# Optimization experiments

Measured on AMD Instinct MI355X. Metric: run time of the kernel, lower is better.

Reference implementation:

```python
import jax, jax.numpy as jnp
import numpy as np
from jax import lax

MAX_MEMORY_LR = 0.2
MIN_MEMORY_DECAY = 0.5
MEMORY_MAX_NORM = 15.0
NORM_EPS = 1e-6

def _inv_sig(x):
    x = max(min(x, 0.999), 0.001)
    return float(np.log(x / (1 - x)))

def setup_inputs() -> dict:
    key = jax.random.key(0)
    k1, k2 = jax.random.split(key)
    B, S, D = 16, 4096, 256
    x = jax.random.normal(k1, (B, S, D), dtype=jnp.float32)
    # xavier_uniform with gain=0.1 on (d_out, d_in)
    limit = 0.1 * float(np.sqrt(6.0 / (D + D)))
    M_init = jax.random.uniform(k2, (D, D), dtype=jnp.float32, minval=-limit, maxval=limit)
    eta_raw = jnp.asarray(_inv_sig(0.05), dtype=jnp.float32)
    alpha_raw = jnp.asarray(_inv_sig(0.9), dtype=jnp.float32)
    return {"x": x, "M_init": M_init, "eta_raw": eta_raw, "alpha_raw": alpha_raw}

def reference(x, M_init, eta_raw, alpha_raw):
    # x: [B, S, d_in], M_init: [d_out, d_in]
    B = x.shape[0]
    eta = jax.nn.sigmoid(eta_raw) * MAX_MEMORY_LR
    alpha = MIN_MEMORY_DECAY + jax.nn.sigmoid(alpha_raw) * (1.0 - MIN_MEMORY_DECAY)
    M0 = jnp.broadcast_to(M_init, (B,) + M_init.shape)

    def step(M, x_t):  # M: [B, d_out, d_in], x_t: [B, d_in]
        out_t = jnp.einsum('boi,bi->bo', M, x_t)  # retrieve
        # key = F.normalize(x_t): x / max(||x||, eps)
        k = x_t / jnp.maximum(jnp.linalg.norm(x_t, axis=-1, keepdims=True), NORM_EPS)
        Mk = jnp.einsum('boi,bi->bo', M, k)
        err = out_t - Mk  # value is out_t (self-generated)
        M_new = alpha * M + eta * err[:, :, None] * k[:, None, :]  # rank-1 delta update
        fro = jnp.sqrt(jnp.sum(M_new * M_new, axis=(-2, -1), keepdims=True))
        scale = jnp.minimum(MEMORY_MAX_NORM / (fro + 1e-6), 1.0)
        return M_new * scale, out_t

    M_final, outs = lax.scan(step, M0, jnp.swapaxes(x, 0, 1))
    return jnp.swapaxes(outs, 0, 1), M_final
```

## Files before the change

### kernel.cpp

```cpp
#include <hip/hip_runtime.h>
#include <hip/hip_bf16.h>
#include <math.h>

typedef float  f32x4  __attribute__((ext_vector_type(4)));
typedef short  bf16x4 __attribute__((ext_vector_type(4)));
typedef __bf16 bfv4   __attribute__((ext_vector_type(4)));

#define B_    16
#define S_    4096
#define D_    256
#define CK_   16
#define NC_   (S_ / CK_)
#define BLOB_ 576
#define W_    8

__device__ __forceinline__ f32x4 mfma_bf16(bf16x4 a, bf16x4 b, f32x4 c) {
#if defined(__has_builtin) && __has_builtin(__builtin_amdgcn_mfma_f32_16x16x16bf16_1k)
    return __builtin_amdgcn_mfma_f32_16x16x16bf16_1k(a, b, c, 0, 0, 0);
#else
    f32x4 d;
    asm("v_mfma_f32_16x16x16_bf16 %0, %1, %2, %3" : "=v"(d) : "v"(a), "v"(b), "v"(c));
    return d;
#endif
}
__device__ __forceinline__ bf16x4 pk4(f32x4 v) {
    bfv4 h;
    h[0] = (__bf16)v[0]; h[1] = (__bf16)v[1]; h[2] = (__bf16)v[2]; h[3] = (__bf16)v[3];
    return __builtin_bit_cast(bf16x4, h);
}
__device__ __forceinline__ f32x4 up4(bf16x4 h) {
    f32x4 r;
    r[0] = __uint_as_float(((unsigned)(unsigned short)h[0]) << 16);
    r[1] = __uint_as_float(((unsigned)(unsigned short)h[1]) << 16);
    r[2] = __uint_as_float(((unsigned)(unsigned short)h[2]) << 16);
    r[3] = __uint_as_float(((unsigned)(unsigned short)h[3]) << 16);
    return r;
}

__global__ __launch_bounds__(64) void ldm_prep(
    const float* __restrict__ x,
    const float* __restrict__ eta_raw,
    const float* __restrict__ alpha_raw,
    unsigned char* __restrict__ blob)
{
    const int lane = threadIdx.x;
    const int b = blockIdx.x >> 8;
    const int c = blockIdx.x & (NC_ - 1);
    const int l15 = lane & 15;
    const int q   = lane >> 4;

    __shared__ float G[256];
    __shared__ float csh[16];
    __shared__ float Tsh[256];

    const float* xp = x + ((size_t)b * S_ + (size_t)c * CK_ + l15) * D_ + q * 4;
    bf16x4 hi[16], lo[16];
    #pragma unroll
    for (int kb = 0; kb < 16; ++kb) {
        f32x4 v = *(const f32x4*)(xp + kb * 16);
        bf16x4 h = pk4(v);
        hi[kb] = h;
        lo[kb] = pk4(v - up4(h));
    }
    f32x4 g1 = {0,0,0,0}, g2 = {0,0,0,0}, g3 = {0,0,0,0};
    #pragma unroll
    for (int kb = 0; kb < 16; ++kb) {
        g1 = mfma_bf16(hi[kb], hi[kb], g1);
        g2 = mfma_bf16(hi[kb], lo[kb], g2);
        g3 = mfma_bf16(lo[kb], hi[kb], g3);
    }
    f32x4 g = (g1 + g2) + g3;
    *(f32x4*)(&G[l15 * 16 + q * 4]) = g;
    __syncthreads();

    const float eta   = 0.2f / (1.0f + expf(-eta_raw[0]));
    const float alpha = 0.5f + 0.5f / (1.0f + expf(-alpha_raw[0]));
    if (lane < 16) {
        float gtt = G[lane * 17];
        float n   = fmaxf(sqrtf(gtt), 1e-6f);
        float inv = 1.0f / n;
        csh[lane] = eta * (1.0f - inv) * inv / alpha;
    }
    __syncthreads();

    if (lane < 16) {
        const int j = lane;
        float cr[16];
        #pragma unroll
        for (int k = 0; k < 16; ++k) cr[k] = csh[k];
        float Tcol[16];
        Tcol[0] = 0.f;
        #pragma unroll
        for (int t = 1; t < 16; ++t) {
            float acc = cr[j] * G[t * 16 + j];
            #pragma unroll
            for (int k = 1; k < 15; ++k)
                if (k < t) acc += cr[k] * G[t * 16 + k] * Tcol[k];
            Tcol[t] = (t > j) ? acc : 0.f;
        }
        #pragma unroll
        for (int t = 0; t < 16; ++t) Tsh[t * 16 + j] = Tcol[t];
    }
    __syncthreads();

    unsigned char* bp = blob + (size_t)(b * NC_ + c) * BLOB_;
    f32x4 tv = *(const f32x4*)(&Tsh[l15 * 16 + q * 4]);
    *(bf16x4*)(bp + (l15 * 16 + q * 4) * 2) = pk4(tv);
    if (lane < 16) ((float*)(bp + 512))[lane] = csh[lane];
}

__global__ __launch_bounds__(512) void ldm_main(
    const float* __restrict__ x,
    const float* __restrict__ Minit,
    const float* __restrict__ alpha_raw,
    const unsigned char* __restrict__ blob,
    float* __restrict__ out)
{
    const int lane   = threadIdx.x & 63;
    const int w      = __builtin_amdgcn_readfirstlane(threadIdx.x >> 6);
    const int batch  = blockIdx.x >> 4;
    const int rowblk = blockIdx.x & 15;
    const int l15    = lane & 15;
    const int q      = lane >> 4;
    const int kcol0  = w * 32 + q * 4;

    __shared__ f32x4 red[2][W_][64];

    const float alpha = 0.5f + 0.5f / (1.0f + expf(-alpha_raw[0]));
    const float a2 = alpha * alpha, a4 = a2 * a2, a8 = a4 * a4, a16 = a8 * a8;
    const float aq = (q == 0) ? 1.f : (q == 1) ? a4 : (q == 2) ? a8 : a8 * a4;
    const f32x4 apow = { aq, aq * alpha, aq * a2, aq * a2 * alpha };

    const int s = l15 - (q << 2);
    bf16x4 IB;
    IB[0] = (s == 0) ? (short)0x3F80 : (short)0;
    IB[1] = (s == 1) ? (short)0x3F80 : (short)0;
    IB[2] = (s == 2) ? (short)0x3F80 : (short)0;
    IB[3] = (s == 3) ? (short)0x3F80 : (short)0;

    const int mrow = rowblk * 16 + l15;
    f32x4 master[2];
    master[0] = *(const f32x4*)(Minit + (size_t)mrow * D_ + kcol0);
    master[1] = *(const f32x4*)(Minit + (size_t)mrow * D_ + kcol0 + 16);

    const float* xb = x + (size_t)batch * S_ * D_;
    const unsigned char* bb0 = blob + (size_t)batch * NC_ * BLOB_;
    float* outp = out + (size_t)batch * S_ * D_ + rowblk * 16 + l15;
    const int tfoff = (l15 * 16 + q * 4) * 2;

    f32x4 XA[2], XB[2];
    bf16x4 TA, TB; f32x4 cA, cB;
    {
        const float* xp = xb + (size_t)l15 * D_ + kcol0;
        XA[0] = *(const f32x4*)(xp);
        XA[1] = *(const f32x4*)(xp + 16);
        TA = *(const bf16x4*)(bb0 + tfoff);
        cA = *(const f32x4*)(bb0 + 512 + q * 16);
    }

    auto body = [&](int c, f32x4 (&XC)[2], f32x4 (&XN)[2],
                    bf16x4& Tc, f32x4& cv, bf16x4& Tn, f32x4& cnv) {
        const int par = c & 1;
        int cx = c + 1; if (cx > NC_ - 1) cx = NC_ - 1;
        {
            const float* xp = xb + ((size_t)cx * CK_ + l15) * D_ + kcol0;
            XN[0] = *(const f32x4*)(xp);
            XN[1] = *(const f32x4*)(xp + 16);
            const unsigned char* bp = bb0 + (size_t)cx * BLOB_;
            Tn = *(const bf16x4*)(bp + tfoff);
            cnv = *(const f32x4*)(bp + 512 + q * 16);
        }
        bf16x4 a0 = pk4(XC[0]), a1 = pk4(XC[1]);
        f32x4 acc = {0,0,0,0};
        acc = mfma_bf16(a0, pk4(master[0]), acc);
        acc = mfma_bf16(a1, pk4(master[1]), acc);
        const f32x4 zz = {0,0,0,0};
        f32x4 t0 = mfma_bf16(a0, IB, zz);
        f32x4 t1 = mfma_bf16(a1, IB, zz);
        red[par][w][lane] = acc;
        __syncthreads();
        f32x4 bbv = red[par][0][lane];
        #pragma unroll
        for (int u = 1; u < W_; ++u) bbv += red[par][u][lane];
        f32x4 d = mfma_bf16(Tc, pk4(bbv), bbv);
        if (w == 0) {
            #pragma unroll
            for (int r = 0; r < 4; ++r)
                outp[(size_t)(c * CK_ + q * 4 + r) * D_] = d[r] * apow[r];
        }
        bf16x4 eup = pk4(d * cv);
        master[0] = mfma_bf16(pk4(t0), eup, master[0]) * a16;
        master[1] = mfma_bf16(pk4(t1), eup, master[1]) * a16;
    };

    for (int c = 0; c < NC_; c += 2) {
        body(c,     XA, XB, TA, cA, TB, cB);
        body(c + 1, XB, XA, TB, cB, TA, cA);
    }

    float* Mout = out + (size_t)B_ * S_ * D_
                + ((size_t)batch * D_ + mrow) * D_;
    *(f32x4*)(Mout + kcol0)      = master[0];
    *(f32x4*)(Mout + kcol0 + 16) = master[1];
}

extern "C" void kernel_launch(void* const* d_in, const int* in_sizes, int n_in,
                              void* d_out, int out_size, void* d_ws, size_t ws_size,
                              hipStream_t stream) {
    const float* x         = (const float*)d_in[0];
    const float* Minit     = (const float*)d_in[1];
    const float* eta_raw   = (const float*)d_in[2];
    const float* alpha_raw = (const float*)d_in[3];
    float* out = (float*)d_out;
    unsigned char* blob = (unsigned char*)d_ws;

    hipLaunchKernelGGL(ldm_prep, dim3(B_ * NC_), dim3(64), 0, stream,
                       x, eta_raw, alpha_raw, blob);
    hipLaunchKernelGGL(ldm_main, dim3(B_ * 16), dim3(512), 0, stream,
                       x, Minit, alpha_raw, blob, out);
}
```

Before: 285.6 us.

## Process two 16-step chunks per barrier using cross-chunk Gram correction

The main kernel now handles pairs of 16-timestep chunks per iteration. The second chunk's retrieval is computed from the pre-update memory and corrected with a precomputed cross-Gram matrix (Gx) times the first chunk's error. This halves the number of block-wide syncs and LDS reductions in the sequential scan. The prep kernel computes Gram, T and cross-Gram per chunk pair, at the cost of a larger blob, more MFMAs on the critical path, and a longer dependent chain per iteration.

After: 273.8 us. -4.1%, faster.

```diff
diff --git a/kernel.cpp b/kernel.cpp
--- a/kernel.cpp
+++ b/kernel.cpp
@@ -11,7 +11,8 @@
 #define D_    256
 #define CK_   16
 #define NC_   (S_ / CK_)
-#define BLOB_ 576
+#define NP_   (NC_ / 2)
+#define PBLOB_ 1664
 #define W_    8
 
 __device__ __forceinline__ f32x4 mfma_bf16(bf16x4 a, bf16x4 b, f32x4 c) {
@@ -44,50 +45,63 @@
     unsigned char* __restrict__ blob)
 {
     const int lane = threadIdx.x;
-    const int b = blockIdx.x >> 8;
-    const int c = blockIdx.x & (NC_ - 1);
+    const int b = blockIdx.x >> 7;
+    const int p = blockIdx.x & (NP_ - 1);
     const int l15 = lane & 15;
     const int q   = lane >> 4;
 
-    __shared__ float G[256];
-    __shared__ float csh[16];
-    __shared__ float Tsh[256];
-
-    const float* xp = x + ((size_t)b * S_ + (size_t)c * CK_ + l15) * D_ + q * 4;
-    bf16x4 hi[16], lo[16];
+    __shared__ float Ga[256], Gb[256], Gxs[256];
+    __shared__ float csh[32];
+    __shared__ float Ts[2][256];
+
+    const float* xa = x + ((size_t)b * S_ + (size_t)p * 32 + l15) * D_ + q * 4;
+    const float* xc = xa + 16 * D_;
+
+    const f32x4 z = {0,0,0,0};
+    f32x4 ga1=z, ga2=z, ga3=z, gb1=z, gb2=z, gb3=z, gx1=z, gx2=z, gx3=z;
+    #pragma unroll 4
+    for (int kb = 0; kb < 16; ++kb) {
+        f32x4 va = *(const f32x4*)(xa + kb * 16);
+        f32x4 vb = *(const f32x4*)(xc + kb * 16);
+        bf16x4 ha = pk4(va), la = pk4(va - up4(ha));
+        bf16x4 hb = pk4(vb), lb = pk4(vb - up4(hb));
+        ga1 = mfma_bf16(ha, ha, ga1);
+        ga2 = mfma_bf16(ha, la, ga2);
+        ga3 = mfma_bf16(la, ha, ga3);
+        gb1 = mfma_bf16(hb, hb, gb1);
+        gb2 = mfma_bf16(hb, lb, gb2);
+        gb3 = mfma_bf16(lb, hb, gb3);
+        gx1 = mfma_bf16(hb, ha, gx1);
+        gx2 = mfma_bf16(hb, la, gx2);
+        gx3 = mfma_bf16(lb, ha, gx3);
+    }
+    f32x4 ga = (ga1 + ga2) + ga3;
+    f32x4 gb = (gb1 + gb2) + gb3;
+    f32x4 gx = (gx1 + gx2) + gx3;
+    *(f32x4*)(&Ga[l15 * 16 + q * 4]) = ga;
+    *(f32x4*)(&Gb[l15 * 16 + q * 4]) = gb;
     #pragma unroll
-    for (int kb = 0; kb < 16; ++kb) {
-        f32x4 v = *(const f32x4*)(xp + kb * 16);
-        bf16x4 h = pk4(v);
-        hi[kb] = h;
-        lo[kb] = pk4(v - up4(h));
-    }
-    f32x4 g1 = {0,0,0,0}, g2 = {0,0,0,0}, g3 = {0,0,0,0};
-    #pragma unroll
-    for (int kb = 0; kb < 16; ++kb) {
-        g1 = mfma_bf16(hi[kb], hi[kb], g1);
-        g2 = mfma_bf16(hi[kb], lo[kb], g2);
-        g3 = mfma_bf16(lo[kb], hi[kb], g3);
-    }
-    f32x4 g = (g1 + g2) + g3;
-    *(f32x4*)(&G[l15 * 16 + q * 4]) = g;
+    for (int r = 0; r < 4; ++r) Gxs[(q * 4 + r) * 16 + l15] = gx[r];
     __syncthreads();
 
     const float eta   = 0.2f / (1.0f + expf(-eta_raw[0]));
     const float alpha = 0.5f + 0.5f / (1.0f + expf(-alpha_raw[0]));
-    if (lane < 16) {
-        float gtt = G[lane * 17];
+    if (lane < 32) {
+        const float* G = (lane < 16) ? Ga : Gb;
+        float gtt = G[l15 * 17];
         float n   = fmaxf(sqrtf(gtt), 1e-6f);
         float inv = 1.0f / n;
         csh[lane] = eta * (1.0f - inv) * inv / alpha;
     }
     __syncthreads();
 
-    if (lane < 16) {
-        const int j = lane;
+    if (lane < 32) {
+        const int j = l15;
+        const float* G  = (lane < 16) ? Ga : Gb;
+        const float* cp = (lane < 16) ? csh : csh + 16;
         float cr[16];
         #pragma unroll
-        for (int k = 0; k < 16; ++k) cr[k] = csh[k];
+        for (int k = 0; k < 16; ++k) cr[k] = cp[k];
         float Tcol[16];
         Tcol[0] = 0.f;
         #pragma unroll
@@ -98,15 +112,18 @@
                 if (k < t) acc += cr[k] * G[t * 16 + k] * Tcol[k];
             Tcol[t] = (t > j) ? acc : 0.f;
         }
+        float* Tsj = Ts[lane >> 4];
         #pragma unroll
-        for (int t = 0; t < 16; ++t) Tsh[t * 16 + j] = Tcol[t];
+        for (int t = 0; t < 16; ++t) Tsj[t * 16 + j] = Tcol[t];
     }
     __syncthreads();
 
-    unsigned char* bp = blob + (size_t)(b * NC_ + c) * BLOB_;
-    f32x4 tv = *(const f32x4*)(&Tsh[l15 * 16 + q * 4]);
-    *(bf16x4*)(bp + (l15 * 16 + q * 4) * 2) = pk4(tv);
-    if (lane < 16) ((float*)(bp + 512))[lane] = csh[lane];
+    unsigned char* bp = blob + (size_t)(b * NP_ + p) * PBLOB_;
+    const int idx = l15 * 16 + q * 4;
+    *(bf16x4*)(bp + idx * 2)        = pk4(*(const f32x4*)(&Ts[0][idx]));
+    *(bf16x4*)(bp + 512 + idx * 2)  = pk4(*(const f32x4*)(&Ts[1][idx]));
+    *(bf16x4*)(bp + 1024 + idx * 2) = pk4(*(const f32x4*)(&Gxs[idx]));
+    if (lane < 32) ((float*)(bp + 1536))[lane] = csh[lane];
 }
 
 __global__ __launch_bounds__(512) void ldm_main(
@@ -124,12 +141,14 @@
     const int q      = lane >> 4;
     const int kcol0  = w * 32 + q * 4;
 
-    __shared__ f32x4 red[2][W_][64];
+    __shared__ f32x4 red[2][2][W_][64];
 
     const float alpha = 0.5f + 0.5f / (1.0f + expf(-alpha_raw[0]));
     const float a2 = alpha * alpha, a4 = a2 * a2, a8 = a4 * a4, a16 = a8 * a8;
+    const float a32 = a16 * a16;
     const float aq = (q == 0) ? 1.f : (q == 1) ? a4 : (q == 2) ? a8 : a8 * a4;
-    const f32x4 apow = { aq, aq * alpha, aq * a2, aq * a2 * alpha };
+    const f32x4 apowA = { aq, aq * alpha, aq * a2, aq * a2 * alpha };
+    const f32x4 apowB = apowA * a16;
 
     const int s = l15 - (q << 2);
     bf16x4 IB;
@@ -144,58 +163,96 @@
     master[1] = *(const f32x4*)(Minit + (size_t)mrow * D_ + kcol0 + 16);
 
     const float* xb = x + (size_t)batch * S_ * D_;
-    const unsigned char* bb0 = blob + (size_t)batch * NC_ * BLOB_;
+    const unsigned char* bb0 = blob + (size_t)batch * NP_ * PBLOB_;
     float* outp = out + (size_t)batch * S_ * D_ + rowblk * 16 + l15;
     const int tfoff = (l15 * 16 + q * 4) * 2;
 
-    f32x4 XA[2], XB[2];
-    bf16x4 TA, TB; f32x4 cA, cB;
+    struct PairBuf {
+        f32x4  Xa[2], Xb[2];
+        bf16x4 Ta, Tb, Gx;
+        f32x4  ca, cb;
+    };
+    PairBuf Abuf, Bbuf;
+
     {
         const float* xp = xb + (size_t)l15 * D_ + kcol0;
-        XA[0] = *(const f32x4*)(xp);
-        XA[1] = *(const f32x4*)(xp + 16);
-        TA = *(const bf16x4*)(bb0 + tfoff);
-        cA = *(const f32x4*)(bb0 + 512 + q * 16);
-    }
-
-    auto body = [&](int c, f32x4 (&XC)[2], f32x4 (&XN)[2],
-                    bf16x4& Tc, f32x4& cv, bf16x4& Tn, f32x4& cnv) {
-        const int par = c & 1;
-        int cx = c + 1; if (cx > NC_ - 1) cx = NC_ - 1;
+        Abuf.Xa[0] = *(const f32x4*)(xp);
+        Abuf.Xa[1] = *(const f32x4*)(xp + 16);
+        Abuf.Xb[0] = *(const f32x4*)(xp + 16 * D_);
+        Abuf.Xb[1] = *(const f32x4*)(xp + 16 * D_ + 16);
+        Abuf.Ta = *(const bf16x4*)(bb0 + tfoff);
+        Abuf.Tb = *(const bf16x4*)(bb0 + 512 + tfoff);
+        Abuf.Gx = *(const bf16x4*)(bb0 + 1024 + tfoff);
+        Abuf.ca = *(const f32x4*)(bb0 + 1536 + q * 16);
+        Abuf.cb = *(const f32x4*)(bb0 + 1600 + q * 16);
+    }
+
+    auto body = [&](int p, PairBuf& cur, PairBuf& nxt) {
+        const int par = p & 1;
+        int px = p + 1; if (px > NP_ - 1) px = NP_ - 1;
         {
-            const float* xp = xb + ((size_t)cx * CK_ + l15) * D_ + kcol0;
-            XN[0] = *(const f32x4*)(xp);
-            XN[1] = *(const f32x4*)(xp + 16);
-            const unsigned char* bp = bb0 + (size_t)cx * BLOB_;
-            Tn = *(const bf16x4*)(bp + tfoff);
-            cnv = *(const f32x4*)(bp + 512 + q * 16);
-        }
-        bf16x4 a0 = pk4(XC[0]), a1 = pk4(XC[1]);
-        f32x4 acc = {0,0,0,0};
-        acc = mfma_bf16(a0, pk4(master[0]), acc);
-        acc = mfma_bf16(a1, pk4(master[1]), acc);
+            const float* xp = xb + ((size_t)px * 32 + l15) * D_ + kcol0;
+            nxt.Xa[0] = *(const f32x4*)(xp);
+            nxt.Xa[1] = *(const f32x4*)(xp + 16);
+            nxt.Xb[0] = *(const f32x4*)(xp + 16 * D_);
+            nxt.Xb[1] = *(const f32x4*)(xp + 16 * D_ + 16);
+            const unsigned char* bp = bb0 + (size_t)px * PBLOB_;
+            nxt.Ta = *(const bf16x4*)(bp + tfoff);
+            nxt.Tb = *(const bf16x4*)(bp + 512 + tfoff);
+            nxt.Gx = *(const bf16x4*)(bp + 1024 + tfoff);
+            nxt.ca = *(const f32x4*)(bp + 1536 + q * 16);
+            nxt.cb = *(const f32x4*)(bp + 1600 + q * 16);
+        }
+        bf16x4 m0 = pk4(master[0]), m1 = pk4(master[1]);
+        bf16x4 a0 = pk4(cur.Xa[0]), a1 = pk4(cur.Xa[1]);
+        bf16x4 b0 = pk4(cur.Xb[0]), b1 = pk4(cur.Xb[1]);
         const f32x4 zz = {0,0,0,0};
-        f32x4 t0 = mfma_bf16(a0, IB, zz);
-        f32x4 t1 = mfma_bf16(a1, IB, zz);
-        red[par][w][lane] = acc;
+        f32x4 acca = mfma_bf16(a0, m0, zz);
+        acca = mfma_bf16(a1, m1, acca);
+        f32x4 accb = mfma_bf16(b0, m0, zz);
+        accb = mfma_bf16(b1, m1, accb);
+        red[par][0][w][lane] = acca;
+        red[par][1][w][lane] = accb;
+        f32x4 t0a = mfma_bf16(a0, IB, zz);
+        f32x4 t1a = mfma_bf16(a1, IB, zz);
+        f32x4 t0b = mfma_bf16(b0, IB, zz);
+        f32x4 t1b = mfma_bf16(b1, IB, zz);
         __syncthreads();
-        f32x4 bbv = red[par][0][lane];
-        #pragma unroll
-        for (int u = 1; u < W_; ++u) bbv += red[par][u][lane];
-        f32x4 d = mfma_bf16(Tc, pk4(bbv), bbv);
+        f32x4 r0 = red[par][0][0][lane], r1 = red[par][0][1][lane];
+        f32x4 r2 = red[par][0][2][lane], r3 = red[par][0][3][lane];
+        f32x4 r4 = red[par][0][4][lane], r5 = red[par][0][5][lane];
+        f32x4 r6 = red[par][0][6][lane], r7 = red[par][0][7][lane];
+        f32x4 bba = ((r0 + r1) + (r2 + r3)) + ((r4 + r5) + (r6 + r7));
+        f32x4 s0 = red[par][1][0][lane], s1 = red[par][1][1][lane];
+        f32x4 s2 = red[par][1][2][lane], s3 = red[par][1][3][lane];
+        f32x4 s4 = red[par][1][4][lane], s5 = red[par][1][5][lane];
+        f32x4 s6 = red[par][1][6][lane], s7 = red[par][1][7][lane];
+        f32x4 bbb = ((s0 + s1) + (s2 + s3)) + ((s4 + s5) + (s6 + s7));
+
+        f32x4 da = mfma_bf16(cur.Ta, pk4(bba), bba);
         if (w == 0) {
             #pragma unroll
             for (int r = 0; r < 4; ++r)
-                outp[(size_t)(c * CK_ + q * 4 + r) * D_] = d[r] * apow[r];
-        }
-        bf16x4 eup = pk4(d * cv);
-        master[0] = mfma_bf16(pk4(t0), eup, master[0]) * a16;
-        master[1] = mfma_bf16(pk4(t1), eup, master[1]) * a16;
+                outp[(size_t)(p * 32 + q * 4 + r) * D_] = da[r] * apowA[r];
+        }
+        bf16x4 ea = pk4(da * cur.ca);
+        f32x4 bbc = mfma_bf16(cur.Gx, ea, bbb);
+        f32x4 db = mfma_bf16(cur.Tb, pk4(bbc), bbc);
+        if (w == 1) {
+            #pragma unroll
+            for (int r = 0; r < 4; ++r)
+                outp[(size_t)(p * 32 + 16 + q * 4 + r) * D_] = db[r] * apowB[r];
+        }
+        bf16x4 eb = pk4(db * cur.cb);
+        master[0] = mfma_bf16(pk4(t0a), ea, master[0]);
+        master[0] = mfma_bf16(pk4(t0b), eb, master[0]) * a32;
+        master[1] = mfma_bf16(pk4(t1a), ea, master[1]);
+        master[1] = mfma_bf16(pk4(t1b), eb, master[1]) * a32;
     };
 
-    for (int c = 0; c < NC_; c += 2) {
-        body(c,     XA, XB, TA, cA, TB, cB);
-        body(c + 1, XB, XA, TB, cB, TA, cA);
+    for (int p = 0; p < NP_; p += 2) {
+        body(p,     Abuf, Bbuf);
+        body(p + 1, Bbuf, Abuf);
     }
 
     float* Mout = out + (size_t)B_ * S_ * D_
@@ -214,7 +271,7 @@
     float* out = (float*)d_out;
     unsigned char* blob = (unsigned char*)d_ws;
 
-    hipLaunchKernelGGL(ldm_prep, dim3(B_ * NC_), dim3(64), 0, stream,
+    hipLaunchKernelGGL(ldm_prep, dim3(B_ * NP_), dim3(64), 0, stream,
                        x, eta_raw, alpha_raw, blob);
     hipLaunchKernelGGL(ldm_main, dim3(B_ * 16), dim3(512), 0, stream,
                        x, Minit, alpha_raw, blob, out);
```
